# Performance work log

Hardware: AMD Instinct MI355X
Metric: run time of the kernel (lower is better)

Reference implementation:

```python
import jax, jax.numpy as jnp
import numpy as np
from jax import lax

B, T, D, H = 2, 2048, 512, 8
HD = D // H
EPS = 1e-5


def _layernorm(x, g, b):
    m = jnp.mean(x, axis=-1, keepdims=True)
    v = jnp.var(x, axis=-1, keepdims=True)
    return (x - m) / jnp.sqrt(v + EPS) * g + b


def setup_inputs() -> dict:
    key = jax.random.key(0)
    ks = jax.random.split(key, 16)
    s = 0.02
    return {
        "x": jax.random.normal(ks[0], (B, T, D), jnp.float32),
        "pe": jax.random.normal(ks[1], (B, T, D), jnp.float32),
        "conv_w": jax.random.normal(ks[2], (D, D, 3), jnp.float32) * s,   # OIH
        "conv_b": jnp.zeros((D,), jnp.float32),
        "in_proj_w": jax.random.normal(ks[3], (3 * D, D), jnp.float32) * s,
        "in_proj_b": jnp.zeros((3 * D,), jnp.float32),
        "out_proj_w": jax.random.normal(ks[4], (D, D), jnp.float32) * s,
        "out_proj_b": jnp.zeros((D,), jnp.float32),
        "ln1_g": jnp.ones((D,), jnp.float32),
        "ln1_b": jnp.zeros((D,), jnp.float32),
        "w1": jax.random.normal(ks[5], (2 * D, D), jnp.float32) * s,
        "b1": jnp.zeros((2 * D,), jnp.float32),
        "w2": jax.random.normal(ks[6], (D, 2 * D), jnp.float32) * s,
        "b2": jnp.zeros((D,), jnp.float32),
        "ln2_g": jnp.ones((D,), jnp.float32),
        "ln2_b": jnp.zeros((D,), jnp.float32),
    }


def reference(x, pe, conv_w, conv_b, in_proj_w, in_proj_b, out_proj_w,
              out_proj_b, ln1_g, ln1_b, w1, b1, w2, b2, ln2_g, ln2_b):
    Bv, Tv, Dv = x.shape
    window = max(Tv // 4, 1)
    half = window // 2
    idx = jnp.arange(Tv)
    blocked = jnp.abs(idx[:, None] - idx[None, :]) > half  # [T, T]
    mask = jnp.where(blocked, -jnp.inf, 0.0).astype(x.dtype)

    # Conv1d on values: x [B,T,D] -> [B,D,T], kernel3 pad1, back to [B,T,D]
    xT = jnp.transpose(x, (0, 2, 1))
    v_in = lax.conv_general_dilated(xT, conv_w, window_strides=(1,),
                                    padding=((1, 1),),
                                    dimension_numbers=("NCH", "OIH", "NCH"))
    v_in = jnp.transpose(v_in + conv_b[None, :, None], (0, 2, 1))

    # MultiheadAttention(q=x, k=x, v=v_in)
    Wq, Wk, Wv = jnp.split(in_proj_w, 3, axis=0)
    bq, bk, bv = jnp.split(in_proj_b, 3, axis=0)
    q = (x @ Wq.T + bq).reshape(Bv, Tv, H, HD).transpose(0, 2, 1, 3)
    k = (x @ Wk.T + bk).reshape(Bv, Tv, H, HD).transpose(0, 2, 1, 3)
    v = (v_in @ Wv.T + bv).reshape(Bv, Tv, H, HD).transpose(0, 2, 1, 3)

    scores = jnp.einsum("bhqd,bhkd->bhqk", q, k) / np.sqrt(HD).astype(x.dtype)
    scores = scores + mask[None, None]
    attn = jax.nn.softmax(scores, axis=-1)
    ctx = jnp.einsum("bhqk,bhkd->bhqd", attn, v)
    ctx = ctx.transpose(0, 2, 1, 3).reshape(Bv, Tv, Dv)
    attn_out = ctx @ out_proj_w.T + out_proj_b

    h = _layernorm(x + attn_out, ln1_g, ln1_b)
    ffn = jax.nn.relu(h @ w1.T + b1) @ w2.T + b2
    return _layernorm(h + ffn, ln2_g, ln2_b)
```

## Files before the change

kernel.cpp:

```cpp
#include <hip/hip_runtime.h>
#include <cstdint>
#include <cstddef>

static constexpr int kT  = 2048;
static constexpr int kD  = 512;
static constexpr int kB  = 2;
static constexpr int kN  = kB * kT;

using short8 = __attribute__((ext_vector_type(8))) short;
using f32x4  = __attribute__((ext_vector_type(4))) float;
typedef unsigned short ushort;

__device__ inline ushort f2bf(float f) {
  uint32_t u = __builtin_bit_cast(uint32_t, f);
  uint32_t r = (u + 0x7FFFu + ((u >> 16) & 1u)) >> 16;
  return (ushort)r;
}

#define GLOAD_LDS16(g, l)                                         \
  __builtin_amdgcn_global_load_lds(                               \
      (const __attribute__((address_space(1))) void*)(g),         \
      (__attribute__((address_space(3))) void*)(l), 16, 0, 0)

struct __align__(16) SmemGemm {
  ushort As[2][64 * 128];
  ushort Bs[2][64 * 128];
};

__global__ __launch_bounds__(256) void prep_kernel(
    const float* __restrict__ x,   const float* __restrict__ ipw,
    const float* __restrict__ opw, const float* __restrict__ w1,
    const float* __restrict__ w2,  const float* __restrict__ cw,
    const float* __restrict__ cb,
    ushort* __restrict__ xb,   ushort* __restrict__ ipwb,
    ushort* __restrict__ opwb, ushort* __restrict__ w1b,
    ushort* __restrict__ w2b,  ushort* __restrict__ wct,
    ushort* __restrict__ acat, float* __restrict__ bvpart)
{
  constexpr int C0 = 524288;
  constexpr int C1 = C0 + 196608;
  constexpr int C2 = C1 + 65536;
  constexpr int C3 = C2 + 131072;
  constexpr int C4 = C3 + 131072;
  constexpr int C5 = C4 + 786432;
  constexpr int C6 = C5 + 786432;
  constexpr int C7 = C6 + 4096;

  auto cast4 = [](const float* in, ushort* out, int u) {
    float4 v = *reinterpret_cast<const float4*>(&in[(size_t)u * 4]);
    ushort o[4] = {f2bf(v.x), f2bf(v.y), f2bf(v.z), f2bf(v.w)};
    *reinterpret_cast<uint2*>(&out[(size_t)u * 4]) =
        *reinterpret_cast<uint2*>(o);
  };

  for (int u = blockIdx.x * 256 + threadIdx.x; u < C7; u += gridDim.x * 256) {
    if (u < C0) {
      cast4(x, xb, u);
    } else if (u < C1) {
      cast4(ipw, ipwb, u - C0);
    } else if (u < C2) {
      cast4(opw, opwb, u - C1);
    } else if (u < C3) {
      cast4(w1, w1b, u - C2);
    } else if (u < C4) {
      cast4(w2, w2b, u - C3);
    } else if (u < C5) {
      int t = u - C4;
      int ti = t >> 9, c = t & 511;
      int tap = ti >> 9, i = ti & 511;
      wct[(size_t)ti * 512 + c] = f2bf(cw[((size_t)c * 512 + i) * 3 + tap]);
    } else if (u < C6) {
      int t = u - C5;
      int m = t / 192, r = t - m * 192;
      int tap = r >> 6, i8 = r & 63;
      int tib = (m & (kT - 1)) + tap - 1;
      ushort ob[8] = {0, 0, 0, 0, 0, 0, 0, 0};
      if (tib >= 0 && tib < kT) {
        const float* src = &x[(size_t)(m + tap - 1) * kD + i8 * 8];
        float4 v0 = *reinterpret_cast<const float4*>(src);
        float4 v1 = *reinterpret_cast<const float4*>(src + 4);
        ob[0] = f2bf(v0.x); ob[1] = f2bf(v0.y); ob[2] = f2bf(v0.z);
        ob[3] = f2bf(v0.w); ob[4] = f2bf(v1.x); ob[5] = f2bf(v1.y);
        ob[6] = f2bf(v1.z); ob[7] = f2bf(v1.w);
      }
      *reinterpret_cast<uint4*>(
          &acat[(size_t)m * (3 * kD) + tap * kD + i8 * 8]) =
          *reinterpret_cast<uint4*>(ob);
    } else {
      int t = u - C6;
      int o = t >> 3, seg = t & 7;
      float s = 0.f;
      const float* wr = &ipw[(size_t)(1024 + o) * kD + seg * 64];
      const float* cr = &cb[seg * 64];
#pragma unroll 8
      for (int c = 0; c < 64; ++c) s = fmaf(wr[c], cr[c], s);
      bvpart[t] = s;
    }
  }
}

template <typename OutT, int RELU>
__device__ void gemm_tile(SmemGemm& S,
    const ushort* __restrict__ A, const ushort* __restrict__ W,
    const float* __restrict__ bias, OutT* __restrict__ C,
    int Nn, int K, int m0, int n0)
{
  const int tid = threadIdx.x;
  const int lane = tid & 63, w = tid >> 6;
  const int wr = w >> 1, wc = w & 1;
  const int fr = lane & 15, g = lane >> 4;

  f32x4 acc[2][2];
#pragma unroll
  for (int i = 0; i < 2; ++i)
#pragma unroll
    for (int j = 0; j < 2; ++j) acc[i][j] = {0.f, 0.f, 0.f, 0.f};

  const ushort* gA[4];
  const ushort* gB[4];
#pragma unroll
  for (int i = 0; i < 4; ++i) {
    int u = i * 256 + tid;
    int row = u >> 4, c = (u & 15) ^ (row & 7);
    gA[i] = A + (size_t)(m0 + row) * K + c * 8;
    gB[i] = W + (size_t)(n0 + row) * K + c * 8;
  }

  auto stage = [&](int buf, int k0) {
#pragma unroll
    for (int i = 0; i < 4; ++i)
      GLOAD_LDS16(gA[i] + k0, &S.As[buf][(i * 256 + w * 64) * 8]);
#pragma unroll
    for (int i = 0; i < 4; ++i)
      GLOAD_LDS16(gB[i] + k0, &S.Bs[buf][(i * 256 + w * 64) * 8]);
  };

  const int nt = K >> 7;
  stage(0, 0);
  for (int t = 0; t < nt; ++t) {
    const int buf = t & 1;
    if (t + 1 < nt) {
      stage(buf ^ 1, (t + 1) << 7);
      asm volatile("s_waitcnt vmcnt(8)" ::: "memory");
    } else {
      asm volatile("s_waitcnt vmcnt(0)" ::: "memory");
    }
    __builtin_amdgcn_s_barrier();
    __builtin_amdgcn_sched_barrier(0);

    short8 av[2][4], bv[2][4];
#pragma unroll
    for (int m = 0; m < 2; ++m)
#pragma unroll
      for (int kc = 0; kc < 4; ++kc) {
        int r = wr * 32 + m * 16 + fr;
        av[m][kc] = *reinterpret_cast<const short8*>(
            &S.As[buf][(r * 16 + ((kc * 4 + g) ^ (r & 7))) * 8]);
      }
#pragma unroll
    for (int n = 0; n < 2; ++n)
#pragma unroll
      for (int kc = 0; kc < 4; ++kc) {
        int r = wc * 32 + n * 16 + fr;
        bv[n][kc] = *reinterpret_cast<const short8*>(
            &S.Bs[buf][(r * 16 + ((kc * 4 + g) ^ (r & 7))) * 8]);
      }
#pragma unroll
    for (int m = 0; m < 2; ++m)
#pragma unroll
      for (int n = 0; n < 2; ++n)
#pragma unroll
        for (int kc = 0; kc < 4; ++kc)
          acc[m][n] = __builtin_amdgcn_mfma_f32_16x16x32_bf16(
              av[m][kc], bv[n][kc], acc[m][n], 0, 0, 0);

    __builtin_amdgcn_sched_barrier(0);
    __builtin_amdgcn_s_barrier();
  }

  float bb[2];
#pragma unroll
  for (int n = 0; n < 2; ++n)
    bb[n] = bias ? bias[n0 + wc * 32 + n * 16 + fr] : 0.f;
#pragma unroll
  for (int m = 0; m < 2; ++m) {
#pragma unroll
    for (int j = 0; j < 4; ++j) {
      int row = m0 + wr * 32 + m * 16 + g * 4 + j;
#pragma unroll
      for (int n = 0; n < 2; ++n) {
        int col = n0 + wc * 32 + n * 16 + fr;
        float v = acc[m][n][j] + bb[n];
        if (RELU) v = fmaxf(v, 0.f);
        if constexpr (sizeof(OutT) == 2)
          C[(size_t)row * Nn + col] = (OutT)f2bf(v);
        else
          C[(size_t)row * Nn + col] = (OutT)v;
      }
    }
  }
}

template <typename OutT, int RELU>
__global__ __launch_bounds__(256) void gemm_bf16(
    const ushort* __restrict__ A, const ushort* __restrict__ W,
    const float* __restrict__ bias, OutT* __restrict__ C, int Nn, int K)
{
  __shared__ SmemGemm S;
  gemm_tile<OutT, RELU>(S, A, W, bias, C, Nn, K,
                        blockIdx.x * 64, blockIdx.y * 64);
}

__global__ __launch_bounds__(256) void wprep_kernel(
    const ushort* __restrict__ ipwb, const ushort* __restrict__ wct,
    ushort* __restrict__ wveff, const float* __restrict__ ipb,
    const float* __restrict__ bvpart, float* __restrict__ bveff)
{
  __shared__ SmemGemm S;
  const int bid = blockIdx.x;
  const int m0 = (bid / 24) * 64, n0 = (bid % 24) * 64;
  gemm_tile<ushort, 0>(S, ipwb + (size_t)1024 * kD, wct, nullptr, wveff,
                       3 * kD, kD, m0, n0);
  if (bid < 2) {
    int o = bid * 256 + threadIdx.x;
    float s = ipb[1024 + o];
#pragma unroll
    for (int e = 0; e < 8; ++e) s += bvpart[o * 8 + e];
    bveff[o] = s;
  }
}

__global__ __launch_bounds__(256) void qkv_kernel(
    const ushort* __restrict__ xb, const ushort* __restrict__ acat,
    const ushort* __restrict__ ipwb, const float* __restrict__ ipb,
    const ushort* __restrict__ wveff, const float* __restrict__ bveff,
    ushort* __restrict__ qkb, ushort* __restrict__ vbb)
{
  __shared__ SmemGemm S;
  const int bid = blockIdx.x;
  if (bid < 1024) {
    gemm_tile<ushort, 0>(S, xb, ipwb, ipb, qkb, 1024, kD,
                         (bid >> 4) * 64, (bid & 15) * 64);
  } else {
    const int t = bid - 1024;
    gemm_tile<ushort, 0>(S, acat, wveff, bveff, vbb, kD, 3 * kD,
                         (t >> 3) * 64, (t & 7) * 64);
  }
}

__global__ __launch_bounds__(256) void attn_mfma(
    const ushort* __restrict__ QK, const ushort* __restrict__ V,
    ushort* __restrict__ Ctx)
{
  constexpr int PAD = 72;
  __shared__ __align__(16) ushort Ks[2][64 * 64];
  __shared__ __align__(16) ushort Vt[2][64][PAD];
  __shared__ __align__(16) ushort Pl[4][16][PAD];
  const int tid = threadIdx.x;
  const int lane = tid & 63, w = tid >> 6;
  const int l15 = lane & 15, g = lane >> 4;
  const int bh = blockIdx.y;
  const int b = bh >> 3, h = bh & 7;
  const int r0 = blockIdx.x * 64;
  const int rowbase = b * kT;
  const int qrow0 = r0 + w * 16;
  const int t_lo = max(r0 - 256, 0);
  const int t_last = min(r0 + 256, kT - 64);
  const int ntiles = ((t_last - t_lo) >> 6) + 1;

  short8 qf[2];
  {
    const size_t qb = (size_t)(rowbase + qrow0 + l15) * 1024 + h * 64 + g * 8;
    qf[0] = *reinterpret_cast<const short8*>(&QK[qb]);
    qf[1] = *reinterpret_cast<const short8*>(&QK[qb + 32]);
  }

  uint4 vreg[2];
  auto issueK = [&](int buf, int j0) {
#pragma unroll
    for (int c = 0; c < 2; ++c) {
      int u = c * 256 + tid;
      int row = u >> 3;
      int col8 = (u & 7) ^ (row & 7);
      const ushort* src =
          &QK[(size_t)(rowbase + j0 + row) * 1024 + 512 + h * 64 + col8 * 8];
      GLOAD_LDS16(src, &Ks[buf][(c * 256 + w * 64) * 8]);
    }
  };
  auto issueV = [&](int j0) {
#pragma unroll
    for (int i = 0; i < 2; ++i)
      vreg[i] = *reinterpret_cast<const uint4*>(
          &V[(size_t)(rowbase + j0 + lane) * 512 + h * 64 + (w + 4 * i) * 8]);
  };
  auto writeV = [&](int buf) {
#pragma unroll
    for (int i = 0; i < 2; ++i) {
      int dg = w + 4 * i;
      ushort tmp[8];
      *reinterpret_cast<uint4*>(tmp) = vreg[i];
#pragma unroll
      for (int e = 0; e < 8; ++e) Vt[buf][dg * 8 + e][lane] = tmp[e];
    }
  };

  f32x4 acc[4];
#pragma unroll
  for (int d = 0; d < 4; ++d) acc[d] = {0.f, 0.f, 0.f, 0.f};
  float mrun[4] = {-1e30f, -1e30f, -1e30f, -1e30f};
  float lrun[4] = {0.f, 0.f, 0.f, 0.f};

  issueK(0, t_lo);
  issueV(t_lo);
  asm volatile("s_waitcnt vmcnt(0)" ::: "memory");
  writeV(0);
  __syncthreads();

  for (int tt = 0; tt < ntiles; ++tt) {
    const int buf = tt & 1;
    const int j0 = t_lo + tt * 64;
    if (tt + 1 < ntiles) {
      issueK(buf ^ 1, j0 + 64);
      issueV(j0 + 64);
    }

    f32x4 s[4];
#pragma unroll
    for (int n = 0; n < 4; ++n) {
      f32x4 z = {0.f, 0.f, 0.f, 0.f};
#pragma unroll
      for (int kc = 0; kc < 2; ++kc) {
        int row = n * 16 + l15;
        int unit = row * 8 + ((kc * 4 + g) ^ (row & 7));
        short8 kb = *reinterpret_cast<const short8*>(&Ks[buf][unit * 8]);
        z = __builtin_amdgcn_mfma_f32_16x16x32_bf16(qf[kc], kb, z, 0, 0, 0);
      }
      s[n] = z;
    }
#pragma unroll
    for (int n = 0; n < 4; ++n)
#pragma unroll
      for (int j = 0; j < 4; ++j) {
        int col = j0 + n * 16 + l15;
        int qr = qrow0 + g * 4 + j;
        int dlt = col - qr;
        float v = s[n][j] * 0.125f;
        s[n][j] = (dlt > 256 || dlt < -256) ? -1e30f : v;
      }
    float pn[4][4];
    float sold[4];
#pragma unroll
    for (int j = 0; j < 4; ++j) {
      float mx = fmaxf(fmaxf(s[0][j], s[1][j]), fmaxf(s[2][j], s[3][j]));
      mx = fmaxf(mx, __shfl_xor(mx, 1));
      mx = fmaxf(mx, __shfl_xor(mx, 2));
      mx = fmaxf(mx, __shfl_xor(mx, 4));
      mx = fmaxf(mx, __shfl_xor(mx, 8));
      float mnew = fmaxf(mrun[j], mx);
      float sc = __expf(mrun[j] - mnew);
      mrun[j] = mnew;
      sold[j] = sc;
      float rs = 0.f;
#pragma unroll
      for (int n = 0; n < 4; ++n) {
        float p = __expf(s[n][j] - mnew);
        pn[n][j] = p;
        rs += p;
      }
      rs += __shfl_xor(rs, 1);
      rs += __shfl_xor(rs, 2);
      rs += __shfl_xor(rs, 4);
      rs += __shfl_xor(rs, 8);
      lrun[j] = lrun[j] * sc + rs;
    }
#pragma unroll
    for (int d = 0; d < 4; ++d)
#pragma unroll
      for (int j = 0; j < 4; ++j) acc[d][j] *= sold[j];
#pragma unroll
    for (int n = 0; n < 4; ++n)
#pragma unroll
      for (int j = 0; j < 4; ++j)
        Pl[w][g * 4 + j][n * 16 + l15] = f2bf(pn[n][j]);
    asm volatile("s_waitcnt lgkmcnt(0)" ::: "memory");
    __builtin_amdgcn_sched_barrier(0);

    short8 pa[2];
    pa[0] = *reinterpret_cast<const short8*>(&Pl[w][l15][g * 8]);
    pa[1] = *reinterpret_cast<const short8*>(&Pl[w][l15][32 + g * 8]);
#pragma unroll
    for (int d = 0; d < 4; ++d) {
#pragma unroll
      for (int kc = 0; kc < 2; ++kc) {
        short8 vb = *reinterpret_cast<const short8*>(
            &Vt[buf][d * 16 + l15][kc * 32 + g * 8]);
        acc[d] = __builtin_amdgcn_mfma_f32_16x16x32_bf16(pa[kc], vb, acc[d], 0, 0, 0);
      }
    }

    if (tt + 1 < ntiles) {
      asm volatile("s_waitcnt vmcnt(0)" ::: "memory");
      writeV(buf ^ 1);
    }
    __syncthreads();
  }

  float inv[4];
#pragma unroll
  for (int j = 0; j < 4; ++j) inv[j] = 1.f / lrun[j];
#pragma unroll
  for (int d = 0; d < 4; ++d)
#pragma unroll
    for (int j = 0; j < 4; ++j) {
      float v = acc[d][j] * inv[j];
      Ctx[(size_t)(rowbase + qrow0 + g * 4 + j) * 512 + h * 64 + d * 16 + l15] =
          f2bf(v);
    }
}

__global__ __launch_bounds__(256) void ln_kernel(
    const float* __restrict__ A, const float* __restrict__ Bq,
    const float* __restrict__ G, const float* __restrict__ Bt,
    float* __restrict__ Out, ushort* __restrict__ OutB)
{
  const int lane = threadIdx.x & 63;
  const int wv = threadIdx.x >> 6;
  const int row = blockIdx.x * 4 + wv;
  const size_t base = (size_t)row * kD + lane * 8;

  float4 a0 = *reinterpret_cast<const float4*>(&A[base]);
  float4 a1 = *reinterpret_cast<const float4*>(&A[base + 4]);
  float4 b0 = *reinterpret_cast<const float4*>(&Bq[base]);
  float4 b1 = *reinterpret_cast<const float4*>(&Bq[base + 4]);
  float x[8] = {a0.x + b0.x, a0.y + b0.y, a0.z + b0.z, a0.w + b0.w,
                a1.x + b1.x, a1.y + b1.y, a1.z + b1.z, a1.w + b1.w};
  float s = 0.f, ss = 0.f;
#pragma unroll
  for (int i = 0; i < 8; ++i) { s += x[i]; ss += x[i] * x[i]; }
#pragma unroll
  for (int o = 1; o < 64; o <<= 1) {
    s += __shfl_xor(s, o, 64);
    ss += __shfl_xor(ss, o, 64);
  }
  const float mean = s * (1.f / kD);
  const float var = ss * (1.f / kD) - mean * mean;
  const float rs = rsqrtf(var + 1e-5f);

  const int c = lane * 8;
  float4 g0 = *reinterpret_cast<const float4*>(&G[c]);
  float4 g1 = *reinterpret_cast<const float4*>(&G[c + 4]);
  float4 t0 = *reinterpret_cast<const float4*>(&Bt[c]);
  float4 t1 = *reinterpret_cast<const float4*>(&Bt[c + 4]);
  float y[8];
  y[0] = (x[0] - mean) * rs * g0.x + t0.x;
  y[1] = (x[1] - mean) * rs * g0.y + t0.y;
  y[2] = (x[2] - mean) * rs * g0.z + t0.z;
  y[3] = (x[3] - mean) * rs * g0.w + t0.w;
  y[4] = (x[4] - mean) * rs * g1.x + t1.x;
  y[5] = (x[5] - mean) * rs * g1.y + t1.y;
  y[6] = (x[6] - mean) * rs * g1.z + t1.z;
  y[7] = (x[7] - mean) * rs * g1.w + t1.w;
  *reinterpret_cast<float4*>(&Out[base]) = {y[0], y[1], y[2], y[3]};
  *reinterpret_cast<float4*>(&Out[base + 4]) = {y[4], y[5], y[6], y[7]};
  if (OutB) {
    ushort ob[8];
#pragma unroll
    for (int i = 0; i < 8; ++i) ob[i] = f2bf(y[i]);
    *reinterpret_cast<uint4*>(&OutB[base]) = *reinterpret_cast<uint4*>(ob);
  }
}

extern "C" void kernel_launch(void* const* d_in, const int* in_sizes, int n_in,
                              void* d_out, int out_size, void* d_ws, size_t ws_size,
                              hipStream_t stream)
{
  const float* x   = (const float*)d_in[0];
  const float* cw  = (const float*)d_in[2];
  const float* cb  = (const float*)d_in[3];
  const float* ipw = (const float*)d_in[4];
  const float* ipb = (const float*)d_in[5];
  const float* opw = (const float*)d_in[6];
  const float* opb = (const float*)d_in[7];
  const float* g1  = (const float*)d_in[8];
  const float* b1n = (const float*)d_in[9];
  const float* w1  = (const float*)d_in[10];
  const float* bb1 = (const float*)d_in[11];
  const float* w2  = (const float*)d_in[12];
  const float* bb2 = (const float*)d_in[13];
  const float* g2  = (const float*)d_in[14];
  const float* b2n = (const float*)d_in[15];
  float* out = (float*)d_out;

  char* p = (char*)d_ws;
  auto take = [&](size_t bytes) {
    char* q = p; p += (bytes + 255) & ~size_t(255); return q;
  };
  ushort* xb    = (ushort*)take((size_t)kN * kD * 2);
  char*  acat_r =          take((size_t)kN * 3 * kD * 2);
  ushort* acat  = (ushort*)acat_r;
  ushort* wct   = (ushort*)take((size_t)3 * kD * kD * 2);
  ushort* wveff = (ushort*)take((size_t)kD * 3 * kD * 2);
  ushort* ipwb  = (ushort*)take((size_t)3 * kD * kD * 2);
  ushort* opwb  = (ushort*)take((size_t)kD * kD * 2);
  ushort* w1b   = (ushort*)take((size_t)2 * kD * kD * 2);
  ushort* w2b   = (ushort*)take((size_t)2 * kD * kD * 2);
  float* bvpart = (float*)take(4096 * 4);
  float* bveff  = (float*)take(512 * 4);
  char*  qk_r   =          take((size_t)kN * 2 * kD * 2);
  ushort* qkb   = (ushort*)qk_r;
  ushort* vbb   = (ushort*)take((size_t)kN * kD * 2);
  ushort* ctx   = (ushort*)take((size_t)kN * kD * 2);
  float* hbuf   = (float*)take((size_t)kN * kD * 4);
  ushort* hb    = (ushort*)take((size_t)kN * kD * 2);
  float* attno  = (float*)acat_r;
  ushort* f1    = (ushort*)qk_r;
  float* f2     = (float*)acat_r;

  dim3 blk(256);
  prep_kernel<<<dim3(2048), blk, 0, stream>>>(
      x, ipw, opw, w1, w2, cw, cb,
      xb, ipwb, opwb, w1b, w2b, wct, acat, bvpart);
  wprep_kernel<<<dim3(192), blk, 0, stream>>>(
      ipwb, wct, wveff, ipb, bvpart, bveff);
  qkv_kernel<<<dim3(1536), blk, 0, stream>>>(
      xb, acat, ipwb, ipb, wveff, bveff, qkb, vbb);
  attn_mfma<<<dim3(kT / 64, kB * 8), blk, 0, stream>>>(qkb, vbb, ctx);
  gemm_bf16<float, 0><<<dim3(kN / 64, kD / 64), blk, 0, stream>>>(
      ctx, opwb, opb, attno, kD, kD);
  ln_kernel<<<dim3(kN / 4), blk, 0, stream>>>(x, attno, g1, b1n, hbuf, hb);
  gemm_bf16<ushort, 1><<<dim3(kN / 64, 1024 / 64), blk, 0, stream>>>(
      hb, w1b, bb1, f1, 1024, kD);
  gemm_bf16<float, 0><<<dim3(kN / 64, kD / 64), blk, 0, stream>>>(
      f1, w2b, bb2, f2, kD, 2 * kD);
  ln_kernel<<<dim3(kN / 4), blk, 0, stream>>>(hbuf, f2, g2, b2n, out, nullptr);
}
```

Before: 205.0 us.

## Fuse LayerNorm into output-proj and FFN2 GEMMs; replace im2col with padded x

Adds a gemm_ln kernel that computes full 512-wide rows (16 rows per block) and applies residual add plus LayerNorm in the epilogue. This removes the two separate ln_kernel launches and the fp32 round-trips of attno/f2. It also drops the 3x im2col acat buffer: it builds a zero-padded bf16 copy of x and reads overlapping rows with stride kD as the conv A operand. The catch is that gemm_ln's 16-row tiles reload the whole weight per block and give lower MFMA reuse than 64x64 tiles.

```diff
diff --git a/kernel.cpp b/kernel.cpp
--- a/kernel.cpp
+++ b/kernel.cpp
@@ -6,6 +6,7 @@
 static constexpr int kD  = 512;
 static constexpr int kB  = 2;
 static constexpr int kN  = kB * kT;
+static constexpr int kTP = kT + 2;
 
 using short8 = __attribute__((ext_vector_type(8))) short;
 using f32x4  = __attribute__((ext_vector_type(4))) float;
@@ -32,19 +33,18 @@
     const float* __restrict__ opw, const float* __restrict__ w1,
     const float* __restrict__ w2,  const float* __restrict__ cw,
     const float* __restrict__ cb,
-    ushort* __restrict__ xb,   ushort* __restrict__ ipwb,
+    ushort* __restrict__ xbp,  ushort* __restrict__ ipwb,
     ushort* __restrict__ opwb, ushort* __restrict__ w1b,
     ushort* __restrict__ w2b,  ushort* __restrict__ wct,
-    ushort* __restrict__ acat, float* __restrict__ bvpart)
-{
-  constexpr int C0 = 524288;
+    float* __restrict__ bvpart)
+{
+  constexpr int C0 = kB * kTP * 64;
   constexpr int C1 = C0 + 196608;
   constexpr int C2 = C1 + 65536;
   constexpr int C3 = C2 + 131072;
   constexpr int C4 = C3 + 131072;
   constexpr int C5 = C4 + 786432;
-  constexpr int C6 = C5 + 786432;
-  constexpr int C7 = C6 + 4096;
+  constexpr int C6 = C5 + 4096;
 
   auto cast4 = [](const float* in, ushort* out, int u) {
     float4 v = *reinterpret_cast<const float4*>(&in[(size_t)u * 4]);
@@ -53,9 +53,21 @@
         *reinterpret_cast<uint2*>(o);
   };
 
-  for (int u = blockIdx.x * 256 + threadIdx.x; u < C7; u += gridDim.x * 256) {
+  for (int u = blockIdx.x * 256 + threadIdx.x; u < C6; u += gridDim.x * 256) {
     if (u < C0) {
-      cast4(x, xb, u);
+      int r = u >> 6, c8 = u & 63;
+      int b = r / kTP, rr = r - b * kTP;
+      ushort ob[8] = {0, 0, 0, 0, 0, 0, 0, 0};
+      if (rr >= 1 && rr <= kT) {
+        const float* src = &x[(size_t)(b * kT + rr - 1) * kD + c8 * 8];
+        float4 v0 = *reinterpret_cast<const float4*>(src);
+        float4 v1 = *reinterpret_cast<const float4*>(src + 4);
+        ob[0] = f2bf(v0.x); ob[1] = f2bf(v0.y); ob[2] = f2bf(v0.z);
+        ob[3] = f2bf(v0.w); ob[4] = f2bf(v1.x); ob[5] = f2bf(v1.y);
+        ob[6] = f2bf(v1.z); ob[7] = f2bf(v1.w);
+      }
+      *reinterpret_cast<uint4*>(&xbp[(size_t)u * 8]) =
+          *reinterpret_cast<uint4*>(ob);
     } else if (u < C1) {
       cast4(ipw, ipwb, u - C0);
     } else if (u < C2) {
@@ -69,25 +81,8 @@
       int ti = t >> 9, c = t & 511;
       int tap = ti >> 9, i = ti & 511;
       wct[(size_t)ti * 512 + c] = f2bf(cw[((size_t)c * 512 + i) * 3 + tap]);
-    } else if (u < C6) {
+    } else {
       int t = u - C5;
-      int m = t / 192, r = t - m * 192;
-      int tap = r >> 6, i8 = r & 63;
-      int tib = (m & (kT - 1)) + tap - 1;
-      ushort ob[8] = {0, 0, 0, 0, 0, 0, 0, 0};
-      if (tib >= 0 && tib < kT) {
-        const float* src = &x[(size_t)(m + tap - 1) * kD + i8 * 8];
-        float4 v0 = *reinterpret_cast<const float4*>(src);
-        float4 v1 = *reinterpret_cast<const float4*>(src + 4);
-        ob[0] = f2bf(v0.x); ob[1] = f2bf(v0.y); ob[2] = f2bf(v0.z);
-        ob[3] = f2bf(v0.w); ob[4] = f2bf(v1.x); ob[5] = f2bf(v1.y);
-        ob[6] = f2bf(v1.z); ob[7] = f2bf(v1.w);
-      }
-      *reinterpret_cast<uint4*>(
-          &acat[(size_t)m * (3 * kD) + tap * kD + i8 * 8]) =
-          *reinterpret_cast<uint4*>(ob);
-    } else {
-      int t = u - C6;
       int o = t >> 3, seg = t & 7;
       float s = 0.f;
       const float* wr = &ipw[(size_t)(1024 + o) * kD + seg * 64];
@@ -101,7 +96,8 @@
 
 template <typename OutT, int RELU>
 __device__ void gemm_tile(SmemGemm& S,
-    const ushort* __restrict__ A, const ushort* __restrict__ W,
+    const ushort* __restrict__ Atile, int lda,
+    const ushort* __restrict__ W,
     const float* __restrict__ bias, OutT* __restrict__ C,
     int Nn, int K, int m0, int n0)
 {
@@ -122,7 +118,7 @@
   for (int i = 0; i < 4; ++i) {
     int u = i * 256 + tid;
     int row = u >> 4, c = (u & 15) ^ (row & 7);
-    gA[i] = A + (size_t)(m0 + row) * K + c * 8;
+    gA[i] = Atile + (size_t)row * lda + c * 8;
     gB[i] = W + (size_t)(n0 + row) * K + c * 8;
   }
 
@@ -207,8 +203,9 @@
     const float* __restrict__ bias, OutT* __restrict__ C, int Nn, int K)
 {
   __shared__ SmemGemm S;
-  gemm_tile<OutT, RELU>(S, A, W, bias, C, Nn, K,
-                        blockIdx.x * 64, blockIdx.y * 64);
+  const int m0 = blockIdx.x * 64;
+  gemm_tile<OutT, RELU>(S, A + (size_t)m0 * K, K, W, bias, C, Nn, K,
+                        m0, blockIdx.y * 64);
 }
 
 __global__ __launch_bounds__(256) void wprep_kernel(
@@ -219,8 +216,8 @@
   __shared__ SmemGemm S;
   const int bid = blockIdx.x;
   const int m0 = (bid / 24) * 64, n0 = (bid % 24) * 64;
-  gemm_tile<ushort, 0>(S, ipwb + (size_t)1024 * kD, wct, nullptr, wveff,
-                       3 * kD, kD, m0, n0);
+  gemm_tile<ushort, 0>(S, ipwb + (size_t)(1024 + m0) * kD, kD, wct,
+                       nullptr, wveff, 3 * kD, kD, m0, n0);
   if (bid < 2) {
     int o = bid * 256 + threadIdx.x;
     float s = ipb[1024 + o];
@@ -231,7 +228,7 @@
 }
 
 __global__ __launch_bounds__(256) void qkv_kernel(
-    const ushort* __restrict__ xb, const ushort* __restrict__ acat,
+    const ushort* __restrict__ xbp,
     const ushort* __restrict__ ipwb, const float* __restrict__ ipb,
     const ushort* __restrict__ wveff, const float* __restrict__ bveff,
     ushort* __restrict__ qkb, ushort* __restrict__ vbb)
@@ -239,12 +236,141 @@
   __shared__ SmemGemm S;
   const int bid = blockIdx.x;
   if (bid < 1024) {
-    gemm_tile<ushort, 0>(S, xb, ipwb, ipb, qkb, 1024, kD,
-                         (bid >> 4) * 64, (bid & 15) * 64);
+    const int m0 = (bid >> 4) * 64;
+    const int bt = m0 >> 11, mi = m0 & (kT - 1);
+    gemm_tile<ushort, 0>(S, xbp + (size_t)(bt * kTP + 1 + mi) * kD, kD,
+                         ipwb, ipb, qkb, 1024, kD, m0, (bid & 15) * 64);
   } else {
     const int t = bid - 1024;
-    gemm_tile<ushort, 0>(S, acat, wveff, bveff, vbb, kD, 3 * kD,
-                         (t >> 3) * 64, (t & 7) * 64);
+    const int m0 = (t >> 3) * 64;
+    const int bt = m0 >> 11, mi = m0 & (kT - 1);
+    gemm_tile<ushort, 0>(S, xbp + (size_t)(bt * kTP + mi) * kD, kD,
+                         wveff, bveff, vbb, kD, 3 * kD, m0, (t & 7) * 64);
+  }
+}
+
+template <int KT, int BF16OUT>
+__global__ __launch_bounds__(256) void gemm_ln(
+    const ushort* __restrict__ A, const ushort* __restrict__ W,
+    const float* __restrict__ bias, const float* __restrict__ res,
+    const float* __restrict__ G, const float* __restrict__ Bt,
+    float* __restrict__ Out, ushort* __restrict__ OutB)
+{
+  constexpr int KTU = KT / 8;
+  constexpr int NCH = KT / 32;
+  __shared__ __align__(16) ushort As[16 * KT];
+  __shared__ __align__(16) ushort Bs[2][512 * 32];
+  const int tid = threadIdx.x;
+  const int lane = tid & 63, w = tid >> 6;
+  const int l15 = lane & 15, g = lane >> 4;
+  const int m0 = blockIdx.x * 16;
+
+  constexpr int AISS = (16 * KTU) / 256;
+  const ushort* gA[AISS];
+#pragma unroll
+  for (int i = 0; i < AISS; ++i) {
+    int idx = i * 256 + tid;
+    int row = idx / KTU, c = idx % KTU;
+    int cs = (c & ~7) | ((c & 7) ^ (row & 7));
+    gA[i] = A + (size_t)(m0 + row) * KT + cs * 8;
+  }
+  const ushort* gB[8];
+#pragma unroll
+  for (int i = 0; i < 8; ++i) {
+    int idx = i * 256 + tid;
+    int col = idx >> 2, uu = idx & 3;
+    gB[i] = W + (size_t)col * KT + uu * 8;
+  }
+
+  auto stageB = [&](int buf, int k0) {
+#pragma unroll
+    for (int i = 0; i < 8; ++i)
+      GLOAD_LDS16(gB[i] + k0, &Bs[buf][(i * 256 + w * 64) * 8]);
+  };
+#pragma unroll
+  for (int i = 0; i < AISS; ++i)
+    GLOAD_LDS16(gA[i], &As[(i * 256 + w * 64) * 8]);
+  stageB(0, 0);
+
+  f32x4 acc[8];
+#pragma unroll
+  for (int f = 0; f < 8; ++f) acc[f] = {0.f, 0.f, 0.f, 0.f};
+
+  for (int t = 0; t < NCH; ++t) {
+    const int buf = t & 1;
+    if (t + 1 < NCH) {
+      stageB(buf ^ 1, (t + 1) * 32);
+      asm volatile("s_waitcnt vmcnt(8)" ::: "memory");
+    } else {
+      asm volatile("s_waitcnt vmcnt(0)" ::: "memory");
+    }
+    __builtin_amdgcn_s_barrier();
+    __builtin_amdgcn_sched_barrier(0);
+
+    short8 a = *reinterpret_cast<const short8*>(
+        &As[(l15 * KTU + ((t * 4 + g) ^ (l15 & 7))) * 8]);
+#pragma unroll
+    for (int f = 0; f < 8; ++f) {
+      int col = w * 128 + f * 16 + l15;
+      short8 bv = *reinterpret_cast<const short8*>(&Bs[buf][(col * 4 + g) * 8]);
+      acc[f] = __builtin_amdgcn_mfma_f32_16x16x32_bf16(a, bv, acc[f], 0, 0, 0);
+    }
+    __builtin_amdgcn_sched_barrier(0);
+    __builtin_amdgcn_s_barrier();
+  }
+
+  float bb[8], gg[8], tt[8];
+#pragma unroll
+  for (int f = 0; f < 8; ++f) {
+    int col = w * 128 + f * 16 + l15;
+    bb[f] = bias[col]; gg[f] = G[col]; tt[f] = Bt[col];
+  }
+#pragma unroll
+  for (int f = 0; f < 8; ++f) {
+    int col = w * 128 + f * 16 + l15;
+#pragma unroll
+    for (int j = 0; j < 4; ++j)
+      acc[f][j] += bb[f] + res[(size_t)(m0 + g * 4 + j) * kD + col];
+  }
+  float sum[4], sq[4];
+#pragma unroll
+  for (int j = 0; j < 4; ++j) {
+    float s = 0.f, q = 0.f;
+#pragma unroll
+    for (int f = 0; f < 8; ++f) { s += acc[f][j]; q += acc[f][j] * acc[f][j]; }
+#pragma unroll
+    for (int o = 1; o < 16; o <<= 1) {
+      s += __shfl_xor(s, o, 64);
+      q += __shfl_xor(q, o, 64);
+    }
+    sum[j] = s; sq[j] = q;
+  }
+  __syncthreads();
+  float* ps = reinterpret_cast<float*>(&Bs[0][0]);
+  float* pq = ps + 64;
+  if (l15 == 0) {
+#pragma unroll
+    for (int j = 0; j < 4; ++j) {
+      ps[w * 16 + g * 4 + j] = sum[j];
+      pq[w * 16 + g * 4 + j] = sq[j];
+    }
+  }
+  __syncthreads();
+#pragma unroll
+  for (int j = 0; j < 4; ++j) {
+    int row = g * 4 + j;
+    float s = ps[row] + ps[16 + row] + ps[32 + row] + ps[48 + row];
+    float q = pq[row] + pq[16 + row] + pq[32 + row] + pq[48 + row];
+    float mean = s * (1.f / kD);
+    float var = q * (1.f / kD) - mean * mean;
+    float rs = rsqrtf(var + 1e-5f);
+#pragma unroll
+    for (int f = 0; f < 8; ++f) {
+      int col = w * 128 + f * 16 + l15;
+      float y = (acc[f][j] - mean) * rs * gg[f] + tt[f];
+      Out[(size_t)(m0 + row) * kD + col] = y;
+      if (BF16OUT) OutB[(size_t)(m0 + row) * kD + col] = f2bf(y);
+    }
   }
 }
 
@@ -416,58 +542,6 @@
       Ctx[(size_t)(rowbase + qrow0 + g * 4 + j) * 512 + h * 64 + d * 16 + l15] =
           f2bf(v);
     }
-}
-
-__global__ __launch_bounds__(256) void ln_kernel(
-    const float* __restrict__ A, const float* __restrict__ Bq,
-    const float* __restrict__ G, const float* __restrict__ Bt,
-    float* __restrict__ Out, ushort* __restrict__ OutB)
-{
-  const int lane = threadIdx.x & 63;
-  const int wv = threadIdx.x >> 6;
-  const int row = blockIdx.x * 4 + wv;
-  const size_t base = (size_t)row * kD + lane * 8;
-
-  float4 a0 = *reinterpret_cast<const float4*>(&A[base]);
-  float4 a1 = *reinterpret_cast<const float4*>(&A[base + 4]);
-  float4 b0 = *reinterpret_cast<const float4*>(&Bq[base]);
-  float4 b1 = *reinterpret_cast<const float4*>(&Bq[base + 4]);
-  float x[8] = {a0.x + b0.x, a0.y + b0.y, a0.z + b0.z, a0.w + b0.w,
-                a1.x + b1.x, a1.y + b1.y, a1.z + b1.z, a1.w + b1.w};
-  float s = 0.f, ss = 0.f;
-#pragma unroll
-  for (int i = 0; i < 8; ++i) { s += x[i]; ss += x[i] * x[i]; }
-#pragma unroll
-  for (int o = 1; o < 64; o <<= 1) {
-    s += __shfl_xor(s, o, 64);
-    ss += __shfl_xor(ss, o, 64);
-  }
-  const float mean = s * (1.f / kD);
-  const float var = ss * (1.f / kD) - mean * mean;
-  const float rs = rsqrtf(var + 1e-5f);
-
-  const int c = lane * 8;
-  float4 g0 = *reinterpret_cast<const float4*>(&G[c]);
-  float4 g1 = *reinterpret_cast<const float4*>(&G[c + 4]);
-  float4 t0 = *reinterpret_cast<const float4*>(&Bt[c]);
-  float4 t1 = *reinterpret_cast<const float4*>(&Bt[c + 4]);
-  float y[8];
-  y[0] = (x[0] - mean) * rs * g0.x + t0.x;
-  y[1] = (x[1] - mean) * rs * g0.y + t0.y;
-  y[2] = (x[2] - mean) * rs * g0.z + t0.z;
-  y[3] = (x[3] - mean) * rs * g0.w + t0.w;
-  y[4] = (x[4] - mean) * rs * g1.x + t1.x;
-  y[5] = (x[5] - mean) * rs * g1.y + t1.y;
-  y[6] = (x[6] - mean) * rs * g1.z + t1.z;
-  y[7] = (x[7] - mean) * rs * g1.w + t1.w;
-  *reinterpret_cast<float4*>(&Out[base]) = {y[0], y[1], y[2], y[3]};
-  *reinterpret_cast<float4*>(&Out[base + 4]) = {y[4], y[5], y[6], y[7]};
-  if (OutB) {
-    ushort ob[8];
-#pragma unroll
-    for (int i = 0; i < 8; ++i) ob[i] = f2bf(y[i]);
-    *reinterpret_cast<uint4*>(&OutB[base]) = *reinterpret_cast<uint4*>(ob);
-  }
 }
 
 extern "C" void kernel_launch(void* const* d_in, const int* in_sizes, int n_in,
@@ -495,9 +569,7 @@
   auto take = [&](size_t bytes) {
     char* q = p; p += (bytes + 255) & ~size_t(255); return q;
   };
-  ushort* xb    = (ushort*)take((size_t)kN * kD * 2);
-  char*  acat_r =          take((size_t)kN * 3 * kD * 2);
-  ushort* acat  = (ushort*)acat_r;
+  ushort* xbp   = (ushort*)take((size_t)kB * kTP * kD * 2);
   ushort* wct   = (ushort*)take((size_t)3 * kD * kD * 2);
   ushort* wveff = (ushort*)take((size_t)kD * 3 * kD * 2);
   ushort* ipwb  = (ushort*)take((size_t)3 * kD * kD * 2);
@@ -512,25 +584,21 @@
   ushort* ctx   = (ushort*)take((size_t)kN * kD * 2);
   float* hbuf   = (float*)take((size_t)kN * kD * 4);
   ushort* hb    = (ushort*)take((size_t)kN * kD * 2);
-  float* attno  = (float*)acat_r;
   ushort* f1    = (ushort*)qk_r;
-  float* f2     = (float*)acat_r;
 
   dim3 blk(256);
   prep_kernel<<<dim3(2048), blk, 0, stream>>>(
       x, ipw, opw, w1, w2, cw, cb,
-      xb, ipwb, opwb, w1b, w2b, wct, acat, bvpart);
+      xbp, ipwb, opwb, w1b, w2b, wct, bvpart);
   wprep_kernel<<<dim3(192), blk, 0, stream>>>(
       ipwb, wct, wveff, ipb, bvpart, bveff);
   qkv_kernel<<<dim3(1536), blk, 0, stream>>>(
-      xb, acat, ipwb, ipb, wveff, bveff, qkb, vbb);
+      xbp, ipwb, ipb, wveff, bveff, qkb, vbb);
   attn_mfma<<<dim3(kT / 64, kB * 8), blk, 0, stream>>>(qkb, vbb, ctx);
-  gemm_bf16<float, 0><<<dim3(kN / 64, kD / 64), blk, 0, stream>>>(
-      ctx, opwb, opb, attno, kD, kD);
-  ln_kernel<<<dim3(kN / 4), blk, 0, stream>>>(x, attno, g1, b1n, hbuf, hb);
+  gemm_ln<512, 1><<<dim3(kN / 16), blk, 0, stream>>>(
+      ctx, opwb, opb, x, g1, b1n, hbuf, hb);
   gemm_bf16<ushort, 1><<<dim3(kN / 64, 1024 / 64), blk, 0, stream>>>(
       hb, w1b, bb1, f1, 1024, kD);
-  gemm_bf16<float, 0><<<dim3(kN / 64, kD / 64), blk, 0, stream>>>(
-      f1, w2b, bb2, f2, kD, 2 * kD);
-  ln_kernel<<<dim3(kN / 4), blk, 0, stream>>>(hbuf, f2, g2, b2n, out, nullptr);
-}
+  gemm_ln<1024, 0><<<dim3(kN / 16), blk, 0, stream>>>(
+      f1, w2b, bb2, hbuf, g2, b2n, out, nullptr);
+}
```

New measurement: 224.5 us. 1.09x slower.
